# Kernel optimization log

Measured on AMD Instinct MI355X. Metric: run time of the kernel, lower is better.

Reference implementation:

```python
import jax, jax.numpy as jnp
import numpy as np
import math

B, S, D = 16, 1, 4096
H, KVH, HD = 32, 8, 128
MAXB, MAXS = 16, 4096
R = H // KVH  # n_rep


def _rope(t, cos, sin):
    # t: [B, S, h, HD]; cos/sin: [S, HD//2]
    tf = t.astype(jnp.float32).reshape(*t.shape[:-1], HD // 2, 2)
    a, b = tf[..., 0], tf[..., 1]
    c = cos[None, :, None, :]
    s = sin[None, :, None, :]
    out = jnp.stack([a * c - b * s, a * s + b * c], axis=-1)
    return out.reshape(t.shape).astype(t.dtype)


def setup_inputs() -> dict:
    key = jax.random.key(0)
    ks = jax.random.split(key, 9)
    scale = 1.0 / math.sqrt(D)
    ang = jax.random.uniform(ks[7], (S, HD // 2), jnp.float32) * (2.0 * np.pi)
    return {
        "x": jax.random.normal(ks[0], (B, S, D), jnp.float32),
        "start_pos": 4095,
        "freqs_cos": jnp.cos(ang),
        "freqs_sin": jnp.sin(ang),
        "cache_k": jax.random.normal(ks[1], (MAXB, MAXS, KVH, HD), jnp.float32),
        "cache_v": jax.random.normal(ks[2], (MAXB, MAXS, KVH, HD), jnp.float32),
        "wq": jax.random.normal(ks[3], (D, H * HD), jnp.float32) * scale,
        "wk": jax.random.normal(ks[4], (D, KVH * HD), jnp.float32) * scale,
        "wv": jax.random.normal(ks[5], (D, KVH * HD), jnp.float32) * scale,
        "wo": jax.random.normal(ks[6], (H * HD, D), jnp.float32) * scale,
    }


def reference(x, start_pos, freqs_cos, freqs_sin, cache_k, cache_v, wq, wk, wv, wo):
    bsz, seqlen, _ = x.shape
    xq = (x @ wq).reshape(bsz, seqlen, H, HD)
    xk = (x @ wk).reshape(bsz, seqlen, KVH, HD)
    xv = (x @ wv).reshape(bsz, seqlen, KVH, HD)
    # rotary embeddings on q and k
    xq = _rope(xq, freqs_cos, freqs_sin)
    xk = _rope(xk, freqs_cos, freqs_sin)
    # KV-cache write (start_pos is a static Python int)
    cache_k = cache_k.at[:bsz, start_pos:start_pos + seqlen].set(xk)
    cache_v = cache_v.at[:bsz, start_pos:start_pos + seqlen].set(xv)
    T = start_pos + seqlen
    keys = cache_k[:bsz, :T]    # [B, T, KVH, HD]
    values = cache_v[:bsz, :T]  # [B, T, KVH, HD]
    # GQA: group q heads as [KVH, R] instead of materializing repeated K/V
    q = xq.reshape(bsz, seqlen, KVH, R, HD)
    scores = jnp.einsum("bsgrd,btgd->bgrst", q, keys) / math.sqrt(HD)
    probs = jax.nn.softmax(scores.astype(jnp.float32), axis=-1).astype(xq.dtype)
    out = jnp.einsum("bgrst,btgd->bsgrd", probs, values)
    out = out.reshape(bsz, seqlen, H * HD)
    return out @ wo
```

## Files before the change

kernel.cpp:

```cpp
#include <hip/hip_runtime.h>
#include <hip/hip_bf16.h>
#include <math.h>

#define B 16
#define D 4096
#define H 32
#define KVH 8
#define HD 128
#define R 4
#define T 4096
#define NQKV 6144
#define NCH_A 32
#define NCH_E 32
#define CT 256
#define NCHUNK 16

#define OFF_QKV   0
#define SZ_QKV    (B*NQKV)
#define OFF_ATTN  (OFF_QKV + SZ_QKV)
#define SZ_ATTN   (B*H*HD)
#define OFF_MLO   (OFF_ATTN + SZ_ATTN)
#define SZ_MLO    (B*KVH*NCHUNK*520)
#define OFF_PART  (OFF_ATTN + SZ_ATTN)

__global__ __launch_bounds__(256) void gemv_qkv(
    const float* __restrict__ x, const float* __restrict__ wq,
    const float* __restrict__ wk, const float* __restrict__ wv,
    float* __restrict__ part) {
  int cb = blockIdx.x;
  int ch = blockIdx.y;
  int d0 = ch * 128;
  __shared__ float xT[128][20];
  for (int i = threadIdx.x; i < 128*B; i += 256) {
    int b = i >> 7;
    int d = i & 127;
    xT[d][b] = x[b*D + d0 + d];
  }
  __syncthreads();
  const float* W; int ncols, colbase, outbase;
  if (cb < 16)      { W = wq; ncols = 4096; colbase = cb*256;      outbase = colbase; }
  else if (cb < 20) { W = wk; ncols = 1024; colbase = (cb-16)*256; outbase = 4096 + colbase; }
  else              { W = wv; ncols = 1024; colbase = (cb-20)*256; outbase = 5120 + colbase; }
  int j = colbase + threadIdx.x;
  const float* wp = W + (size_t)d0*ncols + j;
  float acc[16];
  #pragma unroll
  for (int b = 0; b < 16; ++b) acc[b] = 0.f;
  for (int dd = 0; dd < 128; dd += 8) {
    float w[8];
    #pragma unroll
    for (int u = 0; u < 8; ++u) w[u] = wp[(size_t)u*ncols];
    wp += (size_t)8*ncols;
    #pragma unroll
    for (int u = 0; u < 8; ++u) {
      int d = dd + u;
      #pragma unroll
      for (int bq = 0; bq < 4; ++bq) {
        float4 xb = *(const float4*)&xT[d][bq*4];
        acc[bq*4+0] += w[u]*xb.x;
        acc[bq*4+1] += w[u]*xb.y;
        acc[bq*4+2] += w[u]*xb.z;
        acc[bq*4+3] += w[u]*xb.w;
      }
    }
  }
  int outcol = outbase + threadIdx.x;
  #pragma unroll
  for (int b = 0; b < 16; ++b) {
    part[(size_t)ch*SZ_QKV + b*NQKV + outcol] = acc[b];
  }
}

__global__ __launch_bounds__(256) void reduce_rope(
    const float* __restrict__ part, float* __restrict__ qkv,
    const float* __restrict__ fc, const float* __restrict__ fs) {
  int i = blockIdx.x*256 + threadIdx.x;
  int flat = i*2;
  float2 s = make_float2(0.f, 0.f);
  for (int c = 0; c < NCH_A; ++c) {
    float2 v = *(const float2*)&part[(size_t)c*SZ_QKV + flat];
    s.x += v.x; s.y += v.y;
  }
  int col = flat % NQKV;
  if (col < 5120) {
    int jj = (col & 127) >> 1;
    float c = fc[jj], sn = fs[jj];
    float ox = s.x*c - s.y*sn;
    float oy = s.x*sn + s.y*c;
    if (col < 4096) { ox *= 0.08838834764831845f; oy *= 0.08838834764831845f; }
    s.x = ox; s.y = oy;
  }
  *(float2*)&qkv[flat] = s;
}

__global__ __launch_bounds__(256) void attn_kernel(
    const float* __restrict__ qkv, const float* __restrict__ cache_k,
    const float* __restrict__ cache_v, float* __restrict__ mlo) {
  int chunk = blockIdx.x, g = blockIdx.y, b = blockIdx.z;
  int tid = threadIdx.x, wave = tid >> 6, lane = tid & 63;
  __shared__ float4 q_lds4[4][HD/4];
  __shared__ float4 s_lds4[CT];
  __shared__ float o_lds[4][4][HD];
  for (int i = tid; i < 4*HD; i += 256) {
    int r = i >> 7, d = i & 127;
    ((float*)&q_lds4[r][0])[d] = qkv[b*NQKV + (g*R + r)*HD + d];
  }
  __syncthreads();

  {
    int sub = lane & 7;
    int rloc = lane >> 3;
    #pragma unroll 2
    for (int p = 0; p < 8; ++p) {
      int row = wave*64 + p*8 + rloc;
      int tA = chunk*CT + row;
      const float* kp = (tA == T-1) ? &qkv[b*NQKV + 4096 + g*HD]
                        : &cache_k[(((size_t)b*T + tA)*KVH + g)*HD];
      float4 kreg[4];
      #pragma unroll
      for (int i = 0; i < 4; ++i) kreg[i] = ((const float4*)kp)[i*8 + sub];
      float sA[4] = {0.f,0.f,0.f,0.f};
      #pragma unroll
      for (int i = 0; i < 4; ++i) {
        #pragma unroll
        for (int h = 0; h < 4; ++h) {
          float4 qv = q_lds4[h][i*8 + sub];
          sA[h] += kreg[i].x*qv.x + kreg[i].y*qv.y + kreg[i].z*qv.z + kreg[i].w*qv.w;
        }
      }
      #pragma unroll
      for (int h = 0; h < 4; ++h) {
        sA[h] += __shfl_xor(sA[h], 1);
        sA[h] += __shfl_xor(sA[h], 2);
        sA[h] += __shfl_xor(sA[h], 4);
      }
      if (sub == 0) s_lds4[row] = make_float4(sA[0], sA[1], sA[2], sA[3]);
    }
  }
  __syncthreads();

  {
    int h = wave;
    float v[4]; float m = -1e30f;
    #pragma unroll
    for (int i = 0; i < 4; ++i) {
      v[i] = ((const float*)&s_lds4[lane + i*64])[h];
      m = fmaxf(m, v[i]);
    }
    for (int off = 32; off > 0; off >>= 1) m = fmaxf(m, __shfl_xor(m, off));
    float l = 0.f;
    #pragma unroll
    for (int i = 0; i < 4; ++i) {
      float p = __expf(v[i] - m);
      ((float*)&s_lds4[lane + i*64])[h] = p;
      l += p;
    }
    for (int off = 32; off > 0; off >>= 1) l += __shfl_xor(l, off);
    if (lane == 0) {
      size_t base = ((size_t)(b*KVH + g)*NCHUNK + chunk)*520;
      mlo[base + h] = m;
      mlo[base + 4 + h] = l;
    }
  }
  __syncthreads();

  {
    int sub = lane & 31;
    int rhalf = lane >> 5;
    float4 acc4[4];
    #pragma unroll
    for (int h = 0; h < 4; ++h) acc4[h] = make_float4(0.f,0.f,0.f,0.f);
    int rbase = wave*64;
    #pragma unroll 2
    for (int bt = 0; bt < 8; ++bt) {
      float4 vreg[4];
      #pragma unroll
      for (int i = 0; i < 4; ++i) {
        int tl = rbase + bt*8 + i*2 + rhalf;
        int t = chunk*CT + tl;
        const float* vrow = (t == T-1) ? &qkv[b*NQKV + 5120 + g*HD]
                           : &cache_v[(((size_t)b*T + t)*KVH + g)*HD];
        vreg[i] = *(const float4*)&vrow[sub*4];
      }
      #pragma unroll
      for (int i = 0; i < 4; ++i) {
        int tl = rbase + bt*8 + i*2 + rhalf;
        float4 p = s_lds4[tl];
        acc4[0].x += p.x*vreg[i].x; acc4[0].y += p.x*vreg[i].y;
        acc4[0].z += p.x*vreg[i].z; acc4[0].w += p.x*vreg[i].w;
        acc4[1].x += p.y*vreg[i].x; acc4[1].y += p.y*vreg[i].y;
        acc4[1].z += p.y*vreg[i].z; acc4[1].w += p.y*vreg[i].w;
        acc4[2].x += p.z*vreg[i].x; acc4[2].y += p.z*vreg[i].y;
        acc4[2].z += p.z*vreg[i].z; acc4[2].w += p.z*vreg[i].w;
        acc4[3].x += p.w*vreg[i].x; acc4[3].y += p.w*vreg[i].y;
        acc4[3].z += p.w*vreg[i].z; acc4[3].w += p.w*vreg[i].w;
      }
    }
    #pragma unroll
    for (int h = 0; h < 4; ++h) {
      acc4[h].x += __shfl_xor(acc4[h].x, 32);
      acc4[h].y += __shfl_xor(acc4[h].y, 32);
      acc4[h].z += __shfl_xor(acc4[h].z, 32);
      acc4[h].w += __shfl_xor(acc4[h].w, 32);
    }
    if (rhalf == 0) {
      #pragma unroll
      for (int h = 0; h < 4; ++h)
        *(float4*)&o_lds[wave][h][sub*4] = acc4[h];
    }
  }
  __syncthreads();
  size_t base = ((size_t)(b*KVH + g)*NCHUNK + chunk)*520;
  for (int oi = tid; oi < 512; oi += 256) {
    int h = oi >> 7, d = oi & 127;
    float s = 0.f;
    #pragma unroll
    for (int w = 0; w < 4; ++w) s += o_lds[w][h][d];
    mlo[base + 8 + oi] = s;
  }
}

__global__ __launch_bounds__(128) void combine_kernel(
    const float* __restrict__ mlo, float* __restrict__ attn) {
  int g = blockIdx.x, b = blockIdx.y;
  int d = threadIdx.x;
  #pragma unroll
  for (int h = 0; h < 4; ++h) {
    float mc[NCHUNK], lc[NCHUNK];
    float mg = -1e30f;
    #pragma unroll
    for (int c = 0; c < NCHUNK; ++c) {
      size_t base = ((size_t)(b*KVH + g)*NCHUNK + c)*520;
      mc[c] = mlo[base + h];
      lc[c] = mlo[base + 4 + h];
      mg = fmaxf(mg, mc[c]);
    }
    float lg = 0.f, o = 0.f;
    #pragma unroll
    for (int c = 0; c < NCHUNK; ++c) {
      size_t base = ((size_t)(b*KVH + g)*NCHUNK + c)*520;
      float f = __expf(mc[c] - mg);
      lg += f*lc[c];
      o  += f*mlo[base + 8 + h*HD + d];
    }
    attn[b*D + (g*R + h)*HD + d] = o / lg;
  }
}

__global__ __launch_bounds__(256) void gemv_out(
    const float* __restrict__ attn, const float* __restrict__ wo,
    float* __restrict__ part) {
  int cb = blockIdx.x;
  int ch = blockIdx.y;
  int d0 = ch * 128;
  __shared__ float xT[128][20];
  for (int i = threadIdx.x; i < 128*B; i += 256) {
    int b = i >> 7;
    int d = i & 127;
    xT[d][b] = attn[b*D + d0 + d];
  }
  __syncthreads();
  int j = cb*256 + threadIdx.x;
  const float* wp = wo + (size_t)d0*D + j;
  float acc[16];
  #pragma unroll
  for (int b = 0; b < 16; ++b) acc[b] = 0.f;
  for (int dd = 0; dd < 128; dd += 8) {
    float w[8];
    #pragma unroll
    for (int u = 0; u < 8; ++u) w[u] = wp[(size_t)u*D];
    wp += (size_t)8*D;
    #pragma unroll
    for (int u = 0; u < 8; ++u) {
      int d = dd + u;
      #pragma unroll
      for (int bq = 0; bq < 4; ++bq) {
        float4 xb = *(const float4*)&xT[d][bq*4];
        acc[bq*4+0] += w[u]*xb.x;
        acc[bq*4+1] += w[u]*xb.y;
        acc[bq*4+2] += w[u]*xb.z;
        acc[bq*4+3] += w[u]*xb.w;
      }
    }
  }
  #pragma unroll
  for (int b = 0; b < 16; ++b) {
    part[(size_t)ch*SZ_ATTN + b*D + j] = acc[b];
  }
}

__global__ __launch_bounds__(256) void reduce_part(
    const float* __restrict__ part, float* __restrict__ out, int n, int nch) {
  int i = (blockIdx.x*256 + threadIdx.x)*4;
  if (i >= n) return;
  float4 s = make_float4(0.f,0.f,0.f,0.f);
  for (int c = 0; c < nch; ++c) {
    float4 v = *(const float4*)&part[(size_t)c*n + i];
    s.x += v.x; s.y += v.y; s.z += v.z; s.w += v.w;
  }
  *(float4*)&out[i] = s;
}

extern "C" void kernel_launch(void* const* d_in, const int* in_sizes, int n_in,
                              void* d_out, int out_size, void* d_ws, size_t ws_size,
                              hipStream_t stream) {
  const float* x  = (const float*)d_in[0];
  const float* fc = (const float*)d_in[2];
  const float* fs = (const float*)d_in[3];
  const float* ck = (const float*)d_in[4];
  const float* cv = (const float*)d_in[5];
  const float* wq = (const float*)d_in[6];
  const float* wk = (const float*)d_in[7];
  const float* wv = (const float*)d_in[8];
  const float* wo = (const float*)d_in[9];
  float* out  = (float*)d_out;
  float* ws   = (float*)d_ws;
  float* qkv  = ws + OFF_QKV;
  float* attn = ws + OFF_ATTN;
  float* mlo  = ws + OFF_MLO;
  float* part = ws + OFF_PART;

  gemv_qkv<<<dim3(24, NCH_A), 256, 0, stream>>>(x, wq, wk, wv, part);
  reduce_rope<<<dim3(SZ_QKV/512), 256, 0, stream>>>(part, qkv, fc, fs);
  attn_kernel<<<dim3(NCHUNK, KVH, B), 256, 0, stream>>>(qkv, ck, cv, mlo);
  combine_kernel<<<dim3(KVH, B), 128, 0, stream>>>(mlo, attn);
  gemv_out<<<dim3(16, NCH_E), 256, 0, stream>>>(attn, wo, part);
  reduce_part<<<dim3(SZ_ATTN/1024), 256, 0, stream>>>(part, out, SZ_ATTN, NCH_E);
}
```

Before: 178.4 us.

## Make attention waves independent with per-wave softmax partials

Each wave now computes scores, a local softmax and the PV product for its own 64 tokens. It writes its own (m, l, o) partial directly to global memory, so the block-level syncs and the cross-wave LDS reduction go away. The combine kernel merges 64 sub-chunks per (batch, group) instead of 16. The trade is four times more partial data written and read back, and a longer serial, unrolled-free combine loop in a kernel with only 128 blocks. The larger partial buffer also needs more workspace.

```diff
diff --git a/kernel.cpp b/kernel.cpp
--- a/kernel.cpp
+++ b/kernel.cpp
@@ -13,14 +13,14 @@
 #define NCH_A 32
 #define NCH_E 32
 #define CT 256
-#define NCHUNK 16
+#define NSUB 64
 
 #define OFF_QKV   0
 #define SZ_QKV    (B*NQKV)
 #define OFF_ATTN  (OFF_QKV + SZ_QKV)
 #define SZ_ATTN   (B*H*HD)
 #define OFF_MLO   (OFF_ATTN + SZ_ATTN)
-#define SZ_MLO    (B*KVH*NCHUNK*520)
+#define SZ_MLO    (B*KVH*NSUB*520)
 #define OFF_PART  (OFF_ATTN + SZ_ATTN)
 
 __global__ __launch_bounds__(256) void gemv_qkv(
@@ -99,23 +99,24 @@
   int chunk = blockIdx.x, g = blockIdx.y, b = blockIdx.z;
   int tid = threadIdx.x, wave = tid >> 6, lane = tid & 63;
   __shared__ float4 q_lds4[4][HD/4];
-  __shared__ float4 s_lds4[CT];
-  __shared__ float o_lds[4][4][HD];
+  __shared__ float4 s_lds4[4][64];
   for (int i = tid; i < 4*HD; i += 256) {
     int r = i >> 7, d = i & 127;
     ((float*)&q_lds4[r][0])[d] = qkv[b*NQKV + (g*R + r)*HD + d];
   }
   __syncthreads();
+
+  int t0 = chunk*CT + wave*64;
+  size_t base = ((size_t)(b*KVH + g)*NSUB + (chunk*4 + wave))*520;
 
   {
     int sub = lane & 7;
     int rloc = lane >> 3;
     #pragma unroll 2
     for (int p = 0; p < 8; ++p) {
-      int row = wave*64 + p*8 + rloc;
-      int tA = chunk*CT + row;
-      const float* kp = (tA == T-1) ? &qkv[b*NQKV + 4096 + g*HD]
-                        : &cache_k[(((size_t)b*T + tA)*KVH + g)*HD];
+      int t = t0 + p*8 + rloc;
+      const float* kp = (t == T-1) ? &qkv[b*NQKV + 4096 + g*HD]
+                        : &cache_k[(((size_t)b*T + t)*KVH + g)*HD];
       float4 kreg[4];
       #pragma unroll
       for (int i = 0; i < 4; ++i) kreg[i] = ((const float4*)kp)[i*8 + sub];
@@ -134,35 +135,38 @@
         sA[h] += __shfl_xor(sA[h], 2);
         sA[h] += __shfl_xor(sA[h], 4);
       }
-      if (sub == 0) s_lds4[row] = make_float4(sA[0], sA[1], sA[2], sA[3]);
-    }
-  }
-  __syncthreads();
+      if (sub == 0) s_lds4[wave][p*8 + rloc] = make_float4(sA[0], sA[1], sA[2], sA[3]);
+    }
+  }
 
   {
-    int h = wave;
-    float v[4]; float m = -1e30f;
-    #pragma unroll
-    for (int i = 0; i < 4; ++i) {
-      v[i] = ((const float*)&s_lds4[lane + i*64])[h];
-      m = fmaxf(m, v[i]);
-    }
-    for (int off = 32; off > 0; off >>= 1) m = fmaxf(m, __shfl_xor(m, off));
-    float l = 0.f;
-    #pragma unroll
-    for (int i = 0; i < 4; ++i) {
-      float p = __expf(v[i] - m);
-      ((float*)&s_lds4[lane + i*64])[h] = p;
-      l += p;
-    }
-    for (int off = 32; off > 0; off >>= 1) l += __shfl_xor(l, off);
+    float4 sv = s_lds4[wave][lane];
+    float mh[4] = {sv.x, sv.y, sv.z, sv.w};
+    #pragma unroll
+    for (int h = 0; h < 4; ++h)
+      #pragma unroll
+      for (int off = 32; off > 0; off >>= 1)
+        mh[h] = fmaxf(mh[h], __shfl_xor(mh[h], off));
+    float4 pv;
+    pv.x = __expf(sv.x - mh[0]);
+    pv.y = __expf(sv.y - mh[1]);
+    pv.z = __expf(sv.z - mh[2]);
+    pv.w = __expf(sv.w - mh[3]);
+    s_lds4[wave][lane] = pv;
+    float lh[4] = {pv.x, pv.y, pv.z, pv.w};
+    #pragma unroll
+    for (int h = 0; h < 4; ++h)
+      #pragma unroll
+      for (int off = 32; off > 0; off >>= 1)
+        lh[h] += __shfl_xor(lh[h], off);
     if (lane == 0) {
-      size_t base = ((size_t)(b*KVH + g)*NCHUNK + chunk)*520;
-      mlo[base + h] = m;
-      mlo[base + 4 + h] = l;
-    }
-  }
-  __syncthreads();
+      #pragma unroll
+      for (int h = 0; h < 4; ++h) {
+        mlo[base + h] = mh[h];
+        mlo[base + 4 + h] = lh[h];
+      }
+    }
+  }
 
   {
     int sub = lane & 31;
@@ -170,22 +174,21 @@
     float4 acc4[4];
     #pragma unroll
     for (int h = 0; h < 4; ++h) acc4[h] = make_float4(0.f,0.f,0.f,0.f);
-    int rbase = wave*64;
     #pragma unroll 2
     for (int bt = 0; bt < 8; ++bt) {
       float4 vreg[4];
       #pragma unroll
       for (int i = 0; i < 4; ++i) {
-        int tl = rbase + bt*8 + i*2 + rhalf;
-        int t = chunk*CT + tl;
+        int tl = bt*8 + i*2 + rhalf;
+        int t = t0 + tl;
         const float* vrow = (t == T-1) ? &qkv[b*NQKV + 5120 + g*HD]
                            : &cache_v[(((size_t)b*T + t)*KVH + g)*HD];
         vreg[i] = *(const float4*)&vrow[sub*4];
       }
       #pragma unroll
       for (int i = 0; i < 4; ++i) {
-        int tl = rbase + bt*8 + i*2 + rhalf;
-        float4 p = s_lds4[tl];
+        int tl = bt*8 + i*2 + rhalf;
+        float4 p = s_lds4[wave][tl];
         acc4[0].x += p.x*vreg[i].x; acc4[0].y += p.x*vreg[i].y;
         acc4[0].z += p.x*vreg[i].z; acc4[0].w += p.x*vreg[i].w;
         acc4[1].x += p.y*vreg[i].x; acc4[1].y += p.y*vreg[i].y;
@@ -206,17 +209,8 @@
     if (rhalf == 0) {
       #pragma unroll
       for (int h = 0; h < 4; ++h)
-        *(float4*)&o_lds[wave][h][sub*4] = acc4[h];
-    }
-  }
-  __syncthreads();
-  size_t base = ((size_t)(b*KVH + g)*NCHUNK + chunk)*520;
-  for (int oi = tid; oi < 512; oi += 256) {
-    int h = oi >> 7, d = oi & 127;
-    float s = 0.f;
-    #pragma unroll
-    for (int w = 0; w < 4; ++w) s += o_lds[w][h][d];
-    mlo[base + 8 + oi] = s;
+        *(float4*)&mlo[base + 8 + h*HD + sub*4] = acc4[h];
+    }
   }
 }
 
@@ -224,24 +218,18 @@
     const float* __restrict__ mlo, float* __restrict__ attn) {
   int g = blockIdx.x, b = blockIdx.y;
   int d = threadIdx.x;
+  size_t base0 = (size_t)(b*KVH + g)*NSUB*520;
   #pragma unroll
   for (int h = 0; h < 4; ++h) {
-    float mc[NCHUNK], lc[NCHUNK];
     float mg = -1e30f;
-    #pragma unroll
-    for (int c = 0; c < NCHUNK; ++c) {
-      size_t base = ((size_t)(b*KVH + g)*NCHUNK + c)*520;
-      mc[c] = mlo[base + h];
-      lc[c] = mlo[base + 4 + h];
-      mg = fmaxf(mg, mc[c]);
-    }
+    for (int c = 0; c < NSUB; ++c)
+      mg = fmaxf(mg, mlo[base0 + (size_t)c*520 + h]);
     float lg = 0.f, o = 0.f;
-    #pragma unroll
-    for (int c = 0; c < NCHUNK; ++c) {
-      size_t base = ((size_t)(b*KVH + g)*NCHUNK + c)*520;
-      float f = __expf(mc[c] - mg);
-      lg += f*lc[c];
-      o  += f*mlo[base + 8 + h*HD + d];
+    for (int c = 0; c < NSUB; ++c) {
+      size_t bb = base0 + (size_t)c*520;
+      float f = __expf(mlo[bb + h] - mg);
+      lg += f*mlo[bb + 4 + h];
+      o  += f*mlo[bb + 8 + h*HD + d];
     }
     attn[b*D + (g*R + h)*HD + d] = o / lg;
   }
@@ -322,7 +310,7 @@
 
   gemv_qkv<<<dim3(24, NCH_A), 256, 0, stream>>>(x, wq, wk, wv, part);
   reduce_rope<<<dim3(SZ_QKV/512), 256, 0, stream>>>(part, qkv, fc, fs);
-  attn_kernel<<<dim3(NCHUNK, KVH, B), 256, 0, stream>>>(qkv, ck, cv, mlo);
+  attn_kernel<<<dim3(16, KVH, B), 256, 0, stream>>>(qkv, ck, cv, mlo);
   combine_kernel<<<dim3(KVH, B), 128, 0, stream>>>(mlo, attn);
   gemv_out<<<dim3(16, NCH_E), 256, 0, stream>>>(attn, wo, part);
   reduce_part<<<dim3(SZ_ATTN/1024), 256, 0, stream>>>(part, out, SZ_ATTN, NCH_E);
```

Result: slower. 215.8 us (+21.0%).

## Process two KV heads per attention block for contiguous 1KB cache row reads

Applied to the files above, without the earlier changes.

Each attention block now handles a pair of KV heads (8 query heads), so each wave reads 256 contiguous floats per cache row (two heads) instead of 128. Q values are held in registers per half-wave, and the score reduction moves to a 32-lane shuffle tree. The grid shrinks from 8 to 4 head groups per batch, which halves block count and doubles per-block work. The combine kernel and the partial-result record layout are adjusted to match. The intent is wider, more coalesced HBM access to the KV cache, paid for with more shuffles and fewer blocks in flight.

```diff
diff --git a/kernel.cpp b/kernel.cpp
--- a/kernel.cpp
+++ b/kernel.cpp
@@ -14,13 +14,15 @@
 #define NCH_E 32
 #define CT 256
 #define NCHUNK 16
+#define GP 4
+#define MLOREC 1040
 
 #define OFF_QKV   0
 #define SZ_QKV    (B*NQKV)
 #define OFF_ATTN  (OFF_QKV + SZ_QKV)
 #define SZ_ATTN   (B*H*HD)
 #define OFF_MLO   (OFF_ATTN + SZ_ATTN)
-#define SZ_MLO    (B*KVH*NCHUNK*520)
+#define SZ_MLO    (B*GP*NCHUNK*MLOREC)
 #define OFF_PART  (OFF_ATTN + SZ_ATTN)
 
 __global__ __launch_bounds__(256) void gemv_qkv(
@@ -96,154 +98,163 @@
 __global__ __launch_bounds__(256) void attn_kernel(
     const float* __restrict__ qkv, const float* __restrict__ cache_k,
     const float* __restrict__ cache_v, float* __restrict__ mlo) {
-  int chunk = blockIdx.x, g = blockIdx.y, b = blockIdx.z;
+  int chunk = blockIdx.x, gp = blockIdx.y, b = blockIdx.z;
   int tid = threadIdx.x, wave = tid >> 6, lane = tid & 63;
-  __shared__ float4 q_lds4[4][HD/4];
-  __shared__ float4 s_lds4[CT];
-  __shared__ float o_lds[4][4][HD];
-  for (int i = tid; i < 4*HD; i += 256) {
-    int r = i >> 7, d = i & 127;
-    ((float*)&q_lds4[r][0])[d] = qkv[b*NQKV + (g*R + r)*HD + d];
-  }
-  __syncthreads();
+  int half = lane >> 5, pos = lane & 31;
+  __shared__ float4 q_lds4[8][32];
+  __shared__ float4 s_lds4[CT][2];
+  __shared__ float o_lds[4][8][HD];
+
+  for (int i = tid; i < 8*HD; i += 256) {
+    ((float*)q_lds4)[i] = qkv[b*NQKV + gp*1024 + i];
+  }
+  __syncthreads();
+
+  float4 qreg[4];
+  #pragma unroll
+  for (int h = 0; h < 4; ++h) qreg[h] = q_lds4[half*4 + h][pos];
+
+  const float* ckb = cache_k + (size_t)b*T*1024 + gp*256 + lane*4;
+  const float* cvb = cache_v + (size_t)b*T*1024 + gp*256 + lane*4;
+  const float* ksp = qkv + b*NQKV + 4096 + gp*256 + lane*4;
+  const float* vsp = qkv + b*NQKV + 5120 + gp*256 + lane*4;
+  int t0 = chunk*CT;
 
   {
-    int sub = lane & 7;
-    int rloc = lane >> 3;
-    #pragma unroll 2
-    for (int p = 0; p < 8; ++p) {
-      int row = wave*64 + p*8 + rloc;
-      int tA = chunk*CT + row;
-      const float* kp = (tA == T-1) ? &qkv[b*NQKV + 4096 + g*HD]
-                        : &cache_k[(((size_t)b*T + tA)*KVH + g)*HD];
+    int rbase = wave*64;
+    for (int p = 0; p < 16; ++p) {
       float4 kreg[4];
       #pragma unroll
-      for (int i = 0; i < 4; ++i) kreg[i] = ((const float4*)kp)[i*8 + sub];
-      float sA[4] = {0.f,0.f,0.f,0.f};
+      for (int i = 0; i < 4; ++i) {
+        int t = t0 + rbase + p*4 + i;
+        const float* kp = (t == T-1) ? ksp : ckb + (size_t)t*1024;
+        kreg[i] = *(const float4*)kp;
+      }
+      float sA[4][4];
       #pragma unroll
       for (int i = 0; i < 4; ++i) {
         #pragma unroll
         for (int h = 0; h < 4; ++h) {
-          float4 qv = q_lds4[h][i*8 + sub];
-          sA[h] += kreg[i].x*qv.x + kreg[i].y*qv.y + kreg[i].z*qv.z + kreg[i].w*qv.w;
+          sA[i][h] = kreg[i].x*qreg[h].x + kreg[i].y*qreg[h].y
+                   + kreg[i].z*qreg[h].z + kreg[i].w*qreg[h].w;
         }
       }
       #pragma unroll
-      for (int h = 0; h < 4; ++h) {
-        sA[h] += __shfl_xor(sA[h], 1);
-        sA[h] += __shfl_xor(sA[h], 2);
-        sA[h] += __shfl_xor(sA[h], 4);
-      }
-      if (sub == 0) s_lds4[row] = make_float4(sA[0], sA[1], sA[2], sA[3]);
-    }
-  }
-  __syncthreads();
+      for (int i = 0; i < 4; ++i) {
+        #pragma unroll
+        for (int h = 0; h < 4; ++h) {
+          sA[i][h] += __shfl_xor(sA[i][h], 1);
+          sA[i][h] += __shfl_xor(sA[i][h], 2);
+          sA[i][h] += __shfl_xor(sA[i][h], 4);
+          sA[i][h] += __shfl_xor(sA[i][h], 8);
+          sA[i][h] += __shfl_xor(sA[i][h], 16);
+        }
+      }
+      if (pos == 0) {
+        #pragma unroll
+        for (int i = 0; i < 4; ++i)
+          s_lds4[rbase + p*4 + i][half] = make_float4(sA[i][0], sA[i][1], sA[i][2], sA[i][3]);
+      }
+    }
+  }
+  __syncthreads();
+
+  size_t base = ((size_t)((b*GP + gp)*NCHUNK + chunk))*MLOREC;
 
   {
-    int h = wave;
-    float v[4]; float m = -1e30f;
-    #pragma unroll
-    for (int i = 0; i < 4; ++i) {
-      v[i] = ((const float*)&s_lds4[lane + i*64])[h];
-      m = fmaxf(m, v[i]);
-    }
-    for (int off = 32; off > 0; off >>= 1) m = fmaxf(m, __shfl_xor(m, off));
-    float l = 0.f;
-    #pragma unroll
-    for (int i = 0; i < 4; ++i) {
-      float p = __expf(v[i] - m);
-      ((float*)&s_lds4[lane + i*64])[h] = p;
-      l += p;
-    }
-    for (int off = 32; off > 0; off >>= 1) l += __shfl_xor(l, off);
-    if (lane == 0) {
-      size_t base = ((size_t)(b*KVH + g)*NCHUNK + chunk)*520;
-      mlo[base + h] = m;
-      mlo[base + 4 + h] = l;
+    #pragma unroll
+    for (int jj = 0; jj < 2; ++jj) {
+      int j = wave*2 + jj;
+      float v[4]; float m = -1e30f;
+      #pragma unroll
+      for (int i = 0; i < 4; ++i) {
+        v[i] = ((const float*)&s_lds4[lane + i*64][0])[j];
+        m = fmaxf(m, v[i]);
+      }
+      #pragma unroll
+      for (int off = 32; off > 0; off >>= 1) m = fmaxf(m, __shfl_xor(m, off));
+      float l = 0.f;
+      #pragma unroll
+      for (int i = 0; i < 4; ++i) {
+        float p = __expf(v[i] - m);
+        ((float*)&s_lds4[lane + i*64][0])[j] = p;
+        l += p;
+      }
+      #pragma unroll
+      for (int off = 32; off > 0; off >>= 1) l += __shfl_xor(l, off);
+      if (lane == 0) {
+        mlo[base + j] = m;
+        mlo[base + 8 + j] = l;
+      }
     }
   }
   __syncthreads();
 
   {
-    int sub = lane & 31;
-    int rhalf = lane >> 5;
+    int rbase = wave*64;
     float4 acc4[4];
     #pragma unroll
     for (int h = 0; h < 4; ++h) acc4[h] = make_float4(0.f,0.f,0.f,0.f);
-    int rbase = wave*64;
-    #pragma unroll 2
-    for (int bt = 0; bt < 8; ++bt) {
-      float4 vreg[4];
-      #pragma unroll
-      for (int i = 0; i < 4; ++i) {
-        int tl = rbase + bt*8 + i*2 + rhalf;
-        int t = chunk*CT + tl;
-        const float* vrow = (t == T-1) ? &qkv[b*NQKV + 5120 + g*HD]
-                           : &cache_v[(((size_t)b*T + t)*KVH + g)*HD];
-        vreg[i] = *(const float4*)&vrow[sub*4];
-      }
-      #pragma unroll
-      for (int i = 0; i < 4; ++i) {
-        int tl = rbase + bt*8 + i*2 + rhalf;
-        float4 p = s_lds4[tl];
-        acc4[0].x += p.x*vreg[i].x; acc4[0].y += p.x*vreg[i].y;
-        acc4[0].z += p.x*vreg[i].z; acc4[0].w += p.x*vreg[i].w;
-        acc4[1].x += p.y*vreg[i].x; acc4[1].y += p.y*vreg[i].y;
-        acc4[1].z += p.y*vreg[i].z; acc4[1].w += p.y*vreg[i].w;
-        acc4[2].x += p.z*vreg[i].x; acc4[2].y += p.z*vreg[i].y;
-        acc4[2].z += p.z*vreg[i].z; acc4[2].w += p.z*vreg[i].w;
-        acc4[3].x += p.w*vreg[i].x; acc4[3].y += p.w*vreg[i].y;
-        acc4[3].z += p.w*vreg[i].z; acc4[3].w += p.w*vreg[i].w;
-      }
-    }
-    #pragma unroll
-    for (int h = 0; h < 4; ++h) {
-      acc4[h].x += __shfl_xor(acc4[h].x, 32);
-      acc4[h].y += __shfl_xor(acc4[h].y, 32);
-      acc4[h].z += __shfl_xor(acc4[h].z, 32);
-      acc4[h].w += __shfl_xor(acc4[h].w, 32);
-    }
-    if (rhalf == 0) {
-      #pragma unroll
-      for (int h = 0; h < 4; ++h)
-        *(float4*)&o_lds[wave][h][sub*4] = acc4[h];
-    }
-  }
-  __syncthreads();
-  size_t base = ((size_t)(b*KVH + g)*NCHUNK + chunk)*520;
-  for (int oi = tid; oi < 512; oi += 256) {
-    int h = oi >> 7, d = oi & 127;
-    float s = 0.f;
-    #pragma unroll
-    for (int w = 0; w < 4; ++w) s += o_lds[w][h][d];
-    mlo[base + 8 + oi] = s;
+    for (int bt = 0; bt < 16; ++bt) {
+      float4 vreg[4]; float4 pp[4];
+      #pragma unroll
+      for (int i = 0; i < 4; ++i) {
+        int r = rbase + bt*4 + i;
+        int t = t0 + r;
+        const float* vp = (t == T-1) ? vsp : cvb + (size_t)t*1024;
+        vreg[i] = *(const float4*)vp;
+        pp[i] = s_lds4[r][half];
+      }
+      #pragma unroll
+      for (int i = 0; i < 4; ++i) {
+        acc4[0].x += pp[i].x*vreg[i].x; acc4[0].y += pp[i].x*vreg[i].y;
+        acc4[0].z += pp[i].x*vreg[i].z; acc4[0].w += pp[i].x*vreg[i].w;
+        acc4[1].x += pp[i].y*vreg[i].x; acc4[1].y += pp[i].y*vreg[i].y;
+        acc4[1].z += pp[i].y*vreg[i].z; acc4[1].w += pp[i].y*vreg[i].w;
+        acc4[2].x += pp[i].z*vreg[i].x; acc4[2].y += pp[i].z*vreg[i].y;
+        acc4[2].z += pp[i].z*vreg[i].z; acc4[2].w += pp[i].z*vreg[i].w;
+        acc4[3].x += pp[i].w*vreg[i].x; acc4[3].y += pp[i].w*vreg[i].y;
+        acc4[3].z += pp[i].w*vreg[i].z; acc4[3].w += pp[i].w*vreg[i].w;
+      }
+    }
+    #pragma unroll
+    for (int h = 0; h < 4; ++h)
+      *(float4*)&o_lds[wave][half*4 + h][pos*4] = acc4[h];
+  }
+  __syncthreads();
+
+  for (int oi = tid; oi < 8*HD; oi += 256) {
+    int j = oi >> 7, d = oi & 127;
+    float s = o_lds[0][j][d] + o_lds[1][j][d] + o_lds[2][j][d] + o_lds[3][j][d];
+    mlo[base + 16 + oi] = s;
   }
 }
 
 __global__ __launch_bounds__(128) void combine_kernel(
     const float* __restrict__ mlo, float* __restrict__ attn) {
-  int g = blockIdx.x, b = blockIdx.y;
+  int gp = blockIdx.x, b = blockIdx.y;
   int d = threadIdx.x;
-  #pragma unroll
-  for (int h = 0; h < 4; ++h) {
+  size_t base0 = (size_t)(b*GP + gp)*NCHUNK*MLOREC;
+  #pragma unroll
+  for (int j = 0; j < 8; ++j) {
     float mc[NCHUNK], lc[NCHUNK];
     float mg = -1e30f;
     #pragma unroll
     for (int c = 0; c < NCHUNK; ++c) {
-      size_t base = ((size_t)(b*KVH + g)*NCHUNK + c)*520;
-      mc[c] = mlo[base + h];
-      lc[c] = mlo[base + 4 + h];
+      size_t bb = base0 + (size_t)c*MLOREC;
+      mc[c] = mlo[bb + j];
+      lc[c] = mlo[bb + 8 + j];
       mg = fmaxf(mg, mc[c]);
     }
     float lg = 0.f, o = 0.f;
     #pragma unroll
     for (int c = 0; c < NCHUNK; ++c) {
-      size_t base = ((size_t)(b*KVH + g)*NCHUNK + c)*520;
+      size_t bb = base0 + (size_t)c*MLOREC;
       float f = __expf(mc[c] - mg);
       lg += f*lc[c];
-      o  += f*mlo[base + 8 + h*HD + d];
-    }
-    attn[b*D + (g*R + h)*HD + d] = o / lg;
+      o  += f*mlo[bb + 16 + j*HD + d];
+    }
+    attn[b*D + (gp*8 + j)*HD + d] = o / lg;
   }
 }
 
@@ -322,8 +333,8 @@
 
   gemv_qkv<<<dim3(24, NCH_A), 256, 0, stream>>>(x, wq, wk, wv, part);
   reduce_rope<<<dim3(SZ_QKV/512), 256, 0, stream>>>(part, qkv, fc, fs);
-  attn_kernel<<<dim3(NCHUNK, KVH, B), 256, 0, stream>>>(qkv, ck, cv, mlo);
-  combine_kernel<<<dim3(KVH, B), 128, 0, stream>>>(mlo, attn);
+  attn_kernel<<<dim3(NCHUNK, GP, B), 256, 0, stream>>>(qkv, ck, cv, mlo);
+  combine_kernel<<<dim3(GP, B), 128, 0, stream>>>(mlo, attn);
   gemv_out<<<dim3(16, NCH_E), 256, 0, stream>>>(attn, wo, part);
   reduce_part<<<dim3(SZ_ATTN/1024), 256, 0, stream>>>(part, out, SZ_ATTN, NCH_E);
 }
```

After: 215.3 us. 1.21x slower.
